# Kernel tuning notes

Measured on AMD Instinct MI355X. Metric: run time of the kernel, lower is better.

Reference implementation:

```python
import jax, jax.numpy as jnp
import numpy as np

B, N, S = 8, 8192, 2048
D1, D2 = 128, 256
IN_CH = D1 + D2  # 384
MLP = [256, 128]
BN_EPS = 1e-5


def setup_inputs() -> dict:
    key = jax.random.key(0)
    ks = jax.random.split(key, 12)
    inp = {
        'xyz1': jax.random.normal(ks[0], (B, 3, N), dtype=jnp.float32),
        'xyz2': jax.random.normal(ks[1], (B, 3, S), dtype=jnp.float32),
        'points1': jax.random.normal(ks[2], (B, D1, N), dtype=jnp.float32),
        'points2': jax.random.normal(ks[3], (B, D2, S), dtype=jnp.float32),
    }
    # Conv1d(kernel=1) weights [out, in] + bias, BN gamma/beta per layer
    c_in = IN_CH
    for i, c_out in enumerate(MLP):
        scale = 1.0 / np.sqrt(c_in)
        inp[f'w{i}'] = jax.random.uniform(ks[4 + 2 * i], (c_out, c_in), jnp.float32, -scale, scale)
        inp[f'b{i}'] = jax.random.uniform(ks[5 + 2 * i], (c_out,), jnp.float32, -scale, scale)
        inp[f'g{i}'] = jnp.ones((c_out,), jnp.float32)
        inp[f'be{i}'] = jnp.zeros((c_out,), jnp.float32)
        c_in = c_out
    return inp


def _fp_forward(xyz1, xyz2, points1, points2, params):
    # xyz1: [B,3,N] -> [B,N,3]; xyz2: [B,3,S] -> [B,S,3]
    p1 = jnp.transpose(xyz1, (0, 2, 1))
    p2 = jnp.transpose(xyz2, (0, 2, 1))
    # squared pairwise distances [B,N,S]
    dist = (jnp.sum(p1 * p1, -1)[:, :, None]
            + jnp.sum(p2 * p2, -1)[:, None, :]
            - 2.0 * jnp.einsum('bnc,bsc->bns', p1, p2))
    # 3 smallest distances per query point
    neg_d, idx = jax.lax.top_k(-dist, 3)          # idx: [B,N,3]
    d3 = -neg_d
    recip = 1.0 / (d3 + 1e-8)
    weight = recip / jnp.sum(recip, axis=2, keepdims=True)  # [B,N,3]
    # gather neighbor features: points2 [B,D2,S] -> [B,S,D2]
    feats = jnp.transpose(points2, (0, 2, 1))
    gathered = feats[jnp.arange(feats.shape[0])[:, None, None], idx]  # [B,N,3,D2]
    interp = jnp.einsum('bnkd,bnk->bdn', gathered, weight)            # [B,D2,N]
    x = jnp.concatenate([points1, interp], axis=1)                    # [B,D1+D2,N]
    # Conv1d(k=1) + BatchNorm1d(train-mode batch stats) + ReLU stack
    for w, b, g, be in params:
        x = jnp.einsum('oc,bcn->bon', w, x) + b[None, :, None]
        mean = jnp.mean(x, axis=(0, 2), keepdims=True)
        var = jnp.mean((x - mean) ** 2, axis=(0, 2), keepdims=True)
        x = (x - mean) * jax.lax.rsqrt(var + BN_EPS)
        x = x * g[None, :, None] + be[None, :, None]
        x = jax.nn.relu(x)
    return x


def reference(xyz1, xyz2, points1, points2, w0, b0, g0, be0, w1, b1, g1, be1):
    params = [(w0, b0, g0, be0), (w1, b1, g1, be1)]
    return _fp_forward(xyz1, xyz2, points1, points2, params)
```

## Files before the change

### kernel.cpp

```cpp
#include <hip/hip_runtime.h>

#define NB   8
#define NPT  8192
#define NS   2048
#define ND1  128
#define ND2  256
#define NIN  384
#define NC0  256
#define NC1  128
#define NBN  (NB*NPT)

typedef __bf16 bf16x8 __attribute__((ext_vector_type(8)));
typedef __bf16 bf16x4 __attribute__((ext_vector_type(4)));
typedef float  f32x4  __attribute__((ext_vector_type(4)));

#define SWZ(n, off) ((off) ^ (((n) & 7) << 4))

__global__ __launch_bounds__(256) void knn_kernel(
    const float* __restrict__ xyz1, const float* __restrict__ xyz2,
    int* __restrict__ idx3, float* __restrict__ wgt3)
{
    __shared__ float4 pts[NS];
    __shared__ float md[64][4][3];
    __shared__ int   mi[64][4][3];

    const int b  = blockIdx.x;
    const int qt = blockIdx.y;
    const float* x2 = xyz2 + (size_t)b * 3 * NS;
    for (int s = threadIdx.x; s < NS; s += 256) {
        float x = x2[s], y = x2[NS + s], z = x2[2 * NS + s];
        pts[s] = make_float4(x, y, z, x * x + y * y + z * z);
    }
    __syncthreads();

    const int q    = threadIdx.x & 63;
    const int part = threadIdx.x >> 6;
    const int n    = qt * 64 + q;
    const float* x1 = xyz1 + (size_t)b * 3 * NPT;
    const float px = x1[n], py = x1[NPT + n], pz = x1[2 * NPT + n];
    const float qx = -2.f * px, qy = -2.f * py, qz = -2.f * pz;

    float d0 = 3e38f, d1 = 3e38f, d2 = 3e38f;
    int   i0 = 0, i1 = 0, i2 = 0;
    const int sbeg = part * (NS / 4);
    #pragma unroll 2
    for (int s = sbeg; s < sbeg + NS / 4; ++s) {
        float4 p = pts[s];
        float d = fmaf(qx, p.x, fmaf(qy, p.y, fmaf(qz, p.z, p.w)));
        bool c0 = d < d0, c1 = d < d1, c2 = d < d2;
        i2 = c1 ? i1 : (c2 ? s : i2);
        i1 = c0 ? i0 : (c1 ? s : i1);
        i0 = c0 ? s  : i0;
        d2 = fminf(fmaxf(d, d1), d2);
        d1 = fminf(fmaxf(d, d0), d1);
        d0 = fminf(d, d0);
    }
    md[q][part][0] = d0; md[q][part][1] = d1; md[q][part][2] = d2;
    mi[q][part][0] = i0; mi[q][part][1] = i1; mi[q][part][2] = i2;
    __syncthreads();

    if (threadIdx.x < 64) {
        int hp[4] = {0, 0, 0, 0};
        float rd[3]; int ri[3];
        #pragma unroll
        for (int k = 0; k < 3; ++k) {
            float best = 3.0e38f; int bl = 0;
            #pragma unroll
            for (int l = 0; l < 4; ++l) {
                float dv = md[q][l][hp[l]];
                if (dv < best) { best = dv; bl = l; }
            }
            rd[k] = best; ri[k] = mi[q][bl][hp[bl]]; hp[bl]++;
        }
        const float p1sq = px * px + py * py + pz * pz;
        float r0 = 1.0f / (rd[0] + p1sq + 1e-8f);
        float r1 = 1.0f / (rd[1] + p1sq + 1e-8f);
        float r2 = 1.0f / (rd[2] + p1sq + 1e-8f);
        float inv = 1.0f / (r0 + r1 + r2);
        size_t base = ((size_t)b * NPT + n) * 3;
        idx3[base] = ri[0]; idx3[base + 1] = ri[1]; idx3[base + 2] = ri[2];
        wgt3[base] = r0 * inv; wgt3[base + 1] = r1 * inv; wgt3[base + 2] = r2 * inv;
    }
}

__global__ __launch_bounds__(256) void transpose_p2_kernel(
    const float* __restrict__ p2, __bf16* __restrict__ p2t)
{
    __shared__ float tile[64][65];
    const int b  = blockIdx.x;
    const int ts = (blockIdx.y & 31) * 64;
    const int td = (blockIdx.y >> 5) * 64;
    const int sl = threadIdx.x & 63, dl = threadIdx.x >> 6;
    #pragma unroll
    for (int i = 0; i < 16; ++i)
        tile[dl + 4 * i][sl] = p2[((size_t)b * ND2 + td + dl + 4 * i) * NS + ts + sl];
    __syncthreads();
    const int dl2 = threadIdx.x & 63, sl2 = threadIdx.x >> 6;
    #pragma unroll
    for (int i = 0; i < 16; ++i)
        p2t[((size_t)b * NS + ts + sl2 + 4 * i) * ND2 + td + dl2] =
            (__bf16)tile[dl2][sl2 + 4 * i];
}

__global__ __launch_bounds__(256) void transpose_p1_kernel(
    const float* __restrict__ p1, __bf16* __restrict__ XcP1)
{
    __shared__ float tile[64][65];
    const int b  = blockIdx.x;
    const int tn = (blockIdx.y & 127) * 64;
    const int tc = (blockIdx.y >> 7) * 64;
    const int sl = threadIdx.x & 63, dl = threadIdx.x >> 6;
    #pragma unroll
    for (int i = 0; i < 16; ++i)
        tile[dl + 4 * i][sl] = p1[((size_t)b * ND1 + tc + dl + 4 * i) * NPT + tn + sl];
    __syncthreads();
    const int n_local = threadIdx.x >> 2, c16 = threadIdx.x & 3;
    __bf16* dst = XcP1 + ((size_t)b * NPT + tn + n_local) * ND1 + tc + c16 * 16;
    bf16x8 v0, v1;
    #pragma unroll
    for (int k = 0; k < 8; ++k) {
        v0[k] = (__bf16)tile[c16 * 16 + k][n_local];
        v1[k] = (__bf16)tile[c16 * 16 + 8 + k][n_local];
    }
    *(bf16x8*)dst = v0;
    *(bf16x8*)(dst + 8) = v1;
}

__global__ __launch_bounds__(256) void convert_w_kernel(
    const float* __restrict__ w0, const float* __restrict__ w1,
    __bf16* __restrict__ Wb0, __bf16* __restrict__ Wb1)
{
    const int t = blockIdx.x * 256 + threadIdx.x;
    if (t < NC0 * NIN) Wb0[t] = (__bf16)w0[t];
    if (t < NC1 * NC0) Wb1[t] = (__bf16)w1[t];
}

__global__ __launch_bounds__(512, 4) void gemm0_fused(
    const __bf16* __restrict__ Wb, const __bf16* __restrict__ XcP1,
    const __bf16* __restrict__ p2t,
    const int* __restrict__ idx3, const float* __restrict__ wgt3,
    __bf16* __restrict__ y0, float* __restrict__ sums, float* __restrict__ sumsq)
{
    __shared__ char Bs[64 * ND2 * 2];
    __shared__ float red[2][NC0][2];

    const int tid = threadIdx.x;
    const int bn0 = blockIdx.x * 64;
    const int b   = bn0 / NPT;

    const int ng   = tid >> 3;
    const int part = tid & 7;
    const size_t base3 = (size_t)(bn0 + ng) * 3;
    const int gi0 = idx3[base3], gi1 = idx3[base3 + 1], gi2 = idx3[base3 + 2];
    const float gw0 = wgt3[base3], gw1 = wgt3[base3 + 1], gw2 = wgt3[base3 + 2];
    const __bf16* r0 = p2t + ((size_t)b * NS + gi0) * ND2;
    const __bf16* r1 = p2t + ((size_t)b * NS + gi1) * ND2;
    const __bf16* r2 = p2t + ((size_t)b * NS + gi2) * ND2;

    const int l = tid & 63, w = tid >> 6;
    const int g = l >> 4, lm = l & 15;
    const int ow = w >> 1, nw = w & 1;
    const int o_base = ow * 64;

    f32x4 acc[4][2] = {};

    bf16x8 rawA0, rawA1, rawA2, rawB0, rawB1, rawB2;
    {
        const int d0 = part * 32;
        rawA0 = *(const bf16x8*)(r0 + d0);     rawA1 = *(const bf16x8*)(r1 + d0);
        rawA2 = *(const bf16x8*)(r2 + d0);
        rawB0 = *(const bf16x8*)(r0 + d0 + 8); rawB1 = *(const bf16x8*)(r1 + d0 + 8);
        rawB2 = *(const bf16x8*)(r2 + d0 + 8);
    }

    #pragma unroll
    for (int k0 = 0; k0 < 64; k0 += 32) {
        const int kk = k0 + g * 8;
        bf16x8 af[4], bfr[2];
        #pragma unroll
        for (int m = 0; m < 4; ++m)
            af[m] = *(const bf16x8*)&Wb[(size_t)(o_base + m * 16 + lm) * NIN + kk];
        #pragma unroll
        for (int r = 0; r < 2; ++r) {
            const int n = nw * 32 + r * 16 + lm;
            bfr[r] = *(const bf16x8*)&XcP1[(size_t)(bn0 + n) * ND1 + kk];
        }
        #pragma unroll
        for (int m = 0; m < 4; ++m)
            #pragma unroll
            for (int r = 0; r < 2; ++r)
                acc[m][r] = __builtin_amdgcn_mfma_f32_16x16x32_bf16(af[m], bfr[r], acc[m][r], 0, 0, 0);
    }

    {
        bf16x8 v0, v1;
        #pragma unroll
        for (int j = 0; j < 8; ++j) {
            v0[j] = (__bf16)(gw0 * (float)rawA0[j] + gw1 * (float)rawA1[j] + gw2 * (float)rawA2[j]);
            v1[j] = (__bf16)(gw0 * (float)rawB0[j] + gw1 * (float)rawB1[j] + gw2 * (float)rawB2[j]);
        }
        const int d0 = part * 32;
        *(bf16x8*)(Bs + ng * (ND2 * 2) + SWZ(ng, d0 * 2))       = v0;
        *(bf16x8*)(Bs + ng * (ND2 * 2) + SWZ(ng, (d0 + 8) * 2)) = v1;
    }
    {
        const int d0 = part * 32 + 16;
        rawA0 = *(const bf16x8*)(r0 + d0);     rawA1 = *(const bf16x8*)(r1 + d0);
        rawA2 = *(const bf16x8*)(r2 + d0);
        rawB0 = *(const bf16x8*)(r0 + d0 + 8); rawB1 = *(const bf16x8*)(r1 + d0 + 8);
        rawB2 = *(const bf16x8*)(r2 + d0 + 8);
    }

    #pragma unroll
    for (int k0 = 64; k0 < 128; k0 += 32) {
        const int kk = k0 + g * 8;
        bf16x8 af[4], bfr[2];
        #pragma unroll
        for (int m = 0; m < 4; ++m)
            af[m] = *(const bf16x8*)&Wb[(size_t)(o_base + m * 16 + lm) * NIN + kk];
        #pragma unroll
        for (int r = 0; r < 2; ++r) {
            const int n = nw * 32 + r * 16 + lm;
            bfr[r] = *(const bf16x8*)&XcP1[(size_t)(bn0 + n) * ND1 + kk];
        }
        #pragma unroll
        for (int m = 0; m < 4; ++m)
            #pragma unroll
            for (int r = 0; r < 2; ++r)
                acc[m][r] = __builtin_amdgcn_mfma_f32_16x16x32_bf16(af[m], bfr[r], acc[m][r], 0, 0, 0);
    }

    {
        bf16x8 v0, v1;
        #pragma unroll
        for (int j = 0; j < 8; ++j) {
            v0[j] = (__bf16)(gw0 * (float)rawA0[j] + gw1 * (float)rawA1[j] + gw2 * (float)rawA2[j]);
            v1[j] = (__bf16)(gw0 * (float)rawB0[j] + gw1 * (float)rawB1[j] + gw2 * (float)rawB2[j]);
        }
        const int d0 = part * 32 + 16;
        *(bf16x8*)(Bs + ng * (ND2 * 2) + SWZ(ng, d0 * 2))       = v0;
        *(bf16x8*)(Bs + ng * (ND2 * 2) + SWZ(ng, (d0 + 8) * 2)) = v1;
    }
    __syncthreads();

    #pragma unroll
    for (int k0 = 128; k0 < NIN; k0 += 32) {
        const int kd = k0 - 128 + g * 8;
        bf16x8 af[4], bfr[2];
        #pragma unroll
        for (int m = 0; m < 4; ++m)
            af[m] = *(const bf16x8*)&Wb[(size_t)(o_base + m * 16 + lm) * NIN + k0 + g * 8];
        #pragma unroll
        for (int r = 0; r < 2; ++r) {
            const int n_lds = nw * 32 + r * 16 + lm;
            bfr[r] = *(const bf16x8*)(Bs + n_lds * (ND2 * 2) + SWZ(n_lds, kd * 2));
        }
        #pragma unroll
        for (int m = 0; m < 4; ++m)
            #pragma unroll
            for (int r = 0; r < 2; ++r)
                acc[m][r] = __builtin_amdgcn_mfma_f32_16x16x32_bf16(af[m], bfr[r], acc[m][r], 0, 0, 0);
    }

    #pragma unroll
    for (int m = 0; m < 4; ++m) {
        float s[4] = {0.f, 0.f, 0.f, 0.f}, q[4] = {0.f, 0.f, 0.f, 0.f};
        #pragma unroll
        for (int r = 0; r < 2; ++r) {
            const int n = nw * 32 + r * 16 + lm;
            bf16x4 pk;
            #pragma unroll
            for (int j = 0; j < 4; ++j) {
                float v = acc[m][r][j];
                pk[j] = (__bf16)v;
                s[j] += v; q[j] += v * v;
            }
            *(bf16x4*)&y0[(size_t)(bn0 + n) * NC0 + o_base + m * 16 + g * 4] = pk;
        }
        #pragma unroll
        for (int j = 0; j < 4; ++j) {
            #pragma unroll
            for (int st = 1; st < 16; st <<= 1) {
                s[j] += __shfl_xor(s[j], st);
                q[j] += __shfl_xor(q[j], st);
            }
        }
        if (lm == 0) {
            #pragma unroll
            for (int j = 0; j < 4; ++j) {
                red[0][o_base + m * 16 + g * 4 + j][nw] = s[j];
                red[1][o_base + m * 16 + g * 4 + j][nw] = q[j];
            }
        }
    }
    __syncthreads();
    if (tid < NC0) {
        atomicAdd(&sums[tid],  red[0][tid][0] + red[0][tid][1]);
        atomicAdd(&sumsq[tid], red[1][tid][0] + red[1][tid][1]);
    }
}

__global__ void stats_kernel(
    const float* __restrict__ sums, const float* __restrict__ sumsq,
    const float* __restrict__ g, const float* __restrict__ be,
    float* __restrict__ scale, float* __restrict__ shift, int C)
{
    int c = blockIdx.x * blockDim.x + threadIdx.x;
    if (c < C) {
        const float invN = 1.0f / (float)NBN;
        float mean = sums[c] * invN;
        float var  = sumsq[c] * invN - mean * mean;
        float sc   = g[c] * rsqrtf(var + 1e-5f);
        scale[c] = sc;
        shift[c] = be[c] - mean * sc;
    }
}

__global__ __launch_bounds__(512, 4) void gemm1_mfma(
    const __bf16* __restrict__ Wb, const __bf16* __restrict__ y0,
    const float* __restrict__ scale0, const float* __restrict__ shift0,
    __bf16* __restrict__ y1, float* __restrict__ sums, float* __restrict__ sumsq)
{
    __shared__ float red[2][NC1][4];
    const int tid = threadIdx.x;
    const int l = tid & 63, w = tid >> 6;
    const int g = l >> 4, lm = l & 15;
    const int ow = w >> 2, nw = w & 3;
    const int o_base = ow * 64;
    const int n_base = blockIdx.x * 128 + nw * 32;

    f32x4 acc[4][2] = {};

    for (int k0 = 0; k0 < NC0; k0 += 32) {
        const int kk = k0 + g * 8;
        f32x4 sc0 = *(const f32x4*)&scale0[kk];
        f32x4 sc1 = *(const f32x4*)&scale0[kk + 4];
        f32x4 sh0 = *(const f32x4*)&shift0[kk];
        f32x4 sh1 = *(const f32x4*)&shift0[kk + 4];
        bf16x8 af[4], bfr[2];
        #pragma unroll
        for (int m = 0; m < 4; ++m)
            af[m] = *(const bf16x8*)&Wb[(size_t)(o_base + m * 16 + lm) * NC0 + kk];
        #pragma unroll
        for (int r = 0; r < 2; ++r) {
            bf16x8 raw = *(const bf16x8*)&y0[(size_t)(n_base + r * 16 + lm) * NC0 + kk];
            bf16x8 bb;
            #pragma unroll
            for (int j = 0; j < 4; ++j) {
                bb[j]     = (__bf16)fmaxf((float)raw[j]     * sc0[j] + sh0[j], 0.f);
                bb[j + 4] = (__bf16)fmaxf((float)raw[j + 4] * sc1[j] + sh1[j], 0.f);
            }
            bfr[r] = bb;
        }
        #pragma unroll
        for (int m = 0; m < 4; ++m)
            #pragma unroll
            for (int r = 0; r < 2; ++r)
                acc[m][r] = __builtin_amdgcn_mfma_f32_16x16x32_bf16(af[m], bfr[r], acc[m][r], 0, 0, 0);
    }

    #pragma unroll
    for (int m = 0; m < 4; ++m) {
        float s[4] = {0.f, 0.f, 0.f, 0.f}, q[4] = {0.f, 0.f, 0.f, 0.f};
        #pragma unroll
        for (int r = 0; r < 2; ++r) {
            const int n = n_base + r * 16 + lm;
            #pragma unroll
            for (int j = 0; j < 4; ++j) {
                float v = acc[m][r][j];
                y1[(size_t)(o_base + m * 16 + g * 4 + j) * NBN + n] = (__bf16)v;
                s[j] += v; q[j] += v * v;
            }
        }
        #pragma unroll
        for (int j = 0; j < 4; ++j) {
            #pragma unroll
            for (int st = 1; st < 16; st <<= 1) {
                s[j] += __shfl_xor(s[j], st);
                q[j] += __shfl_xor(q[j], st);
            }
        }
        if (lm == 0) {
            #pragma unroll
            for (int j = 0; j < 4; ++j) {
                red[0][o_base + m * 16 + g * 4 + j][nw] = s[j];
                red[1][o_base + m * 16 + g * 4 + j][nw] = q[j];
            }
        }
    }
    __syncthreads();
    if (tid < NC1) {
        atomicAdd(&sums[tid],  red[0][tid][0] + red[0][tid][1] + red[0][tid][2] + red[0][tid][3]);
        atomicAdd(&sumsq[tid], red[1][tid][0] + red[1][tid][1] + red[1][tid][2] + red[1][tid][3]);
    }
}

__global__ __launch_bounds__(256) void bnout_kernel(
    const __bf16* __restrict__ y1, const float* __restrict__ scale1,
    const float* __restrict__ shift1, float* __restrict__ out)
{
    const size_t t = (size_t)blockIdx.x * 256 + threadIdx.x;
    const size_t e = t * 8;
    const int n = (int)(e & (NPT - 1));
    const int o = (int)((e >> 13) & (NC1 - 1));
    const int b = (int)(e >> 20);
    bf16x8 v = *(const bf16x8*)&y1[(size_t)o * NBN + (size_t)b * NPT + n];
    const float s = scale1[o], sh = shift1[o];
    f32x4 r0, r1;
    #pragma unroll
    for (int j = 0; j < 4; ++j) {
        r0[j] = fmaxf((float)v[j]     * s + sh, 0.f);
        r1[j] = fmaxf((float)v[j + 4] * s + sh, 0.f);
    }
    *(f32x4*)&out[e]     = r0;
    *(f32x4*)&out[e + 4] = r1;
}

extern "C" void kernel_launch(void* const* d_in, const int* in_sizes, int n_in,
                              void* d_out, int out_size, void* d_ws, size_t ws_size,
                              hipStream_t stream)
{
    const float* xyz1    = (const float*)d_in[0];
    const float* xyz2    = (const float*)d_in[1];
    const float* points1 = (const float*)d_in[2];
    const float* points2 = (const float*)d_in[3];
    const float* w0  = (const float*)d_in[4];
    const float* g0  = (const float*)d_in[6];
    const float* be0 = (const float*)d_in[7];
    const float* w1  = (const float*)d_in[8];
    const float* g1  = (const float*)d_in[10];
    const float* be1 = (const float*)d_in[11];

    char* ws = (char*)d_ws;
    size_t off = 0;
    int*    idx3 = (int*)(ws + off);    off += (size_t)NBN * 3 * 4;
    float*  wgt3 = (float*)(ws + off);  off += (size_t)NBN * 3 * 4;
    __bf16* XcP1 = (__bf16*)(ws + off); off += (size_t)NBN * ND1 * 2;
    __bf16* y0   = (__bf16*)(ws + off); off += (size_t)NBN * NC0 * 2;
    __bf16* y1   = (__bf16*)(ws + off); off += (size_t)NC1 * NBN * 2;
    __bf16* p2t  = (__bf16*)(ws + off); off += (size_t)NB * NS * ND2 * 2;
    __bf16* Wb0  = (__bf16*)(ws + off); off += (size_t)NC0 * NIN * 2;
    __bf16* Wb1  = (__bf16*)(ws + off); off += (size_t)NC1 * NC0 * 2;
    float*  stats = (float*)(ws + off);
    float* sums0  = stats;        float* sumsq0 = stats + 256;
    float* sums1  = stats + 512;  float* sumsq1 = stats + 640;
    float* scale0 = stats + 768;  float* shift0 = stats + 1024;
    float* scale1 = stats + 1280; float* shift1 = stats + 1408;

    hipMemsetAsync(stats, 0, 768 * 4, stream);

    convert_w_kernel   <<<dim3(NC0 * NIN / 256), 256, 0, stream>>>(w0, w1, Wb0, Wb1);
    transpose_p2_kernel<<<dim3(NB, 128), 256, 0, stream>>>(points2, p2t);
    transpose_p1_kernel<<<dim3(NB, 256), 256, 0, stream>>>(points1, XcP1);
    knn_kernel         <<<dim3(NB, 128), 256, 0, stream>>>(xyz1, xyz2, idx3, wgt3);
    gemm0_fused        <<<dim3(NBN / 64), 512, 0, stream>>>(
        Wb0, XcP1, p2t, idx3, wgt3, y0, sums0, sumsq0);
    stats_kernel       <<<1, 256, 0, stream>>>(sums0, sumsq0, g0, be0, scale0, shift0, NC0);
    gemm1_mfma         <<<dim3(NBN / 128), 512, 0, stream>>>(Wb1, y0, scale0, shift0, y1, sums1, sumsq1);
    stats_kernel       <<<1, 128, 0, stream>>>(sums1, sumsq1, g1, be1, scale1, shift1, NC1);
    bnout_kernel       <<<dim3(NBN * NC1 / 8 / 256), 256, 0, stream>>>(y1, scale1, shift1, (float*)d_out);
}
```

Before: 327.9 us.

## Pre-pack weights and activations into MFMA fragment-order layouts for coalesced loads

Weights, the transposed points1 and the layer-0 output are now written in a packed tile layout that matches the MFMA 16x16x32 operand fragment order. Each wavefront's fragment load then reads one contiguous 1KB chunk instead of 16 strided rows. The aim is to cut scattered global accesses and cache-line waste in both GEMMs. The cost is more complex index arithmetic in the producer kernels, and the packed y0 stores become more scattered.

```diff
diff --git a/kernel.cpp b/kernel.cpp
--- a/kernel.cpp
+++ b/kernel.cpp
@@ -15,6 +15,7 @@
 typedef float  f32x4  __attribute__((ext_vector_type(4)));
 
 #define SWZ(n, off) ((off) ^ (((n) & 7) << 4))
+
 
 __global__ __launch_bounds__(256) void knn_kernel(
     const float* __restrict__ xyz1, const float* __restrict__ xyz2,
@@ -103,7 +104,7 @@
 }
 
 __global__ __launch_bounds__(256) void transpose_p1_kernel(
-    const float* __restrict__ p1, __bf16* __restrict__ XcP1)
+    const float* __restrict__ p1, __bf16* __restrict__ Bp)
 {
     __shared__ float tile[64][65];
     const int b  = blockIdx.x;
@@ -115,37 +116,55 @@
         tile[dl + 4 * i][sl] = p1[((size_t)b * ND1 + tc + dl + 4 * i) * NPT + tn + sl];
     __syncthreads();
     const int n_local = threadIdx.x >> 2, c16 = threadIdx.x & 3;
-    __bf16* dst = XcP1 + ((size_t)b * NPT + tn + n_local) * ND1 + tc + c16 * 16;
     bf16x8 v0, v1;
     #pragma unroll
     for (int k = 0; k < 8; ++k) {
         v0[k] = (__bf16)tile[c16 * 16 + k][n_local];
         v1[k] = (__bf16)tile[c16 * 16 + 8 + k][n_local];
     }
-    *(bf16x8*)dst = v0;
-    *(bf16x8*)(dst + 8) = v1;
-}
-
-__global__ __launch_bounds__(256) void convert_w_kernel(
+    const int n16 = (int)(((size_t)b * NPT + tn + n_local) >> 4);
+    const int lm  = n_local & 15;
+    const int kc  = (tc >> 5) + (c16 >> 1);
+    const int g0  = (c16 & 1) * 2;
+    __bf16* base = Bp + (((size_t)n16 * 4 + kc) * 64 + lm) * 8;
+    *(bf16x8*)(base + g0 * 128)       = v0;
+    *(bf16x8*)(base + (g0 + 1) * 128) = v1;
+}
+
+__global__ __launch_bounds__(64) void pack_w_kernel(
     const float* __restrict__ w0, const float* __restrict__ w1,
-    __bf16* __restrict__ Wb0, __bf16* __restrict__ Wb1)
-{
-    const int t = blockIdx.x * 256 + threadIdx.x;
-    if (t < NC0 * NIN) Wb0[t] = (__bf16)w0[t];
-    if (t < NC1 * NC0) Wb1[t] = (__bf16)w1[t];
+    __bf16* __restrict__ Ap0, __bf16* __restrict__ Ap1)
+{
+    const int o  = blockIdx.x;
+    const int k8 = threadIdx.x;
+    if (k8 < 48) {
+        const float* src = w0 + (size_t)o * NIN + k8 * 8;
+        bf16x8 v;
+        #pragma unroll
+        for (int e = 0; e < 8; ++e) v[e] = (__bf16)src[e];
+        *(bf16x8*)&Ap0[((((o >> 4) * 12 + (k8 >> 2)) * 4 + (k8 & 3)) * 16 + (o & 15)) * 8] = v;
+    }
+    if (o < NC1 && k8 < 32) {
+        const float* src = w1 + (size_t)o * NC0 + k8 * 8;
+        bf16x8 v;
+        #pragma unroll
+        for (int e = 0; e < 8; ++e) v[e] = (__bf16)src[e];
+        *(bf16x8*)&Ap1[((((o >> 4) * 8 + (k8 >> 2)) * 4 + (k8 & 3)) * 16 + (o & 15)) * 8] = v;
+    }
 }
 
 __global__ __launch_bounds__(512, 4) void gemm0_fused(
-    const __bf16* __restrict__ Wb, const __bf16* __restrict__ XcP1,
+    const __bf16* __restrict__ Ap0, const __bf16* __restrict__ Bp,
     const __bf16* __restrict__ p2t,
     const int* __restrict__ idx3, const float* __restrict__ wgt3,
-    __bf16* __restrict__ y0, float* __restrict__ sums, float* __restrict__ sumsq)
+    __bf16* __restrict__ Yp, float* __restrict__ sums, float* __restrict__ sumsq)
 {
     __shared__ char Bs[64 * ND2 * 2];
     __shared__ float red[2][NC0][2];
 
     const int tid = threadIdx.x;
-    const int bn0 = blockIdx.x * 64;
+    const int bx  = blockIdx.x;
+    const int bn0 = bx * 64;
     const int b   = bn0 / NPT;
 
     const int ng   = tid >> 3;
@@ -175,16 +194,14 @@
 
     #pragma unroll
     for (int k0 = 0; k0 < 64; k0 += 32) {
-        const int kk = k0 + g * 8;
+        const int kc = k0 >> 5;
         bf16x8 af[4], bfr[2];
         #pragma unroll
         for (int m = 0; m < 4; ++m)
-            af[m] = *(const bf16x8*)&Wb[(size_t)(o_base + m * 16 + lm) * NIN + kk];
-        #pragma unroll
-        for (int r = 0; r < 2; ++r) {
-            const int n = nw * 32 + r * 16 + lm;
-            bfr[r] = *(const bf16x8*)&XcP1[(size_t)(bn0 + n) * ND1 + kk];
-        }
+            af[m] = *(const bf16x8*)&Ap0[(((ow * 4 + m) * 12 + kc) * 64 + l) * 8];
+        #pragma unroll
+        for (int r = 0; r < 2; ++r)
+            bfr[r] = *(const bf16x8*)&Bp[((((size_t)bx * 4 + nw * 2 + r) * 4 + kc) * 64 + l) * 8];
         #pragma unroll
         for (int m = 0; m < 4; ++m)
             #pragma unroll
@@ -213,16 +230,14 @@
 
     #pragma unroll
     for (int k0 = 64; k0 < 128; k0 += 32) {
-        const int kk = k0 + g * 8;
+        const int kc = k0 >> 5;
         bf16x8 af[4], bfr[2];
         #pragma unroll
         for (int m = 0; m < 4; ++m)
-            af[m] = *(const bf16x8*)&Wb[(size_t)(o_base + m * 16 + lm) * NIN + kk];
-        #pragma unroll
-        for (int r = 0; r < 2; ++r) {
-            const int n = nw * 32 + r * 16 + lm;
-            bfr[r] = *(const bf16x8*)&XcP1[(size_t)(bn0 + n) * ND1 + kk];
-        }
+            af[m] = *(const bf16x8*)&Ap0[(((ow * 4 + m) * 12 + kc) * 64 + l) * 8];
+        #pragma unroll
+        for (int r = 0; r < 2; ++r)
+            bfr[r] = *(const bf16x8*)&Bp[((((size_t)bx * 4 + nw * 2 + r) * 4 + kc) * 64 + l) * 8];
         #pragma unroll
         for (int m = 0; m < 4; ++m)
             #pragma unroll
@@ -245,11 +260,12 @@
 
     #pragma unroll
     for (int k0 = 128; k0 < NIN; k0 += 32) {
+        const int kc = k0 >> 5;
         const int kd = k0 - 128 + g * 8;
         bf16x8 af[4], bfr[2];
         #pragma unroll
         for (int m = 0; m < 4; ++m)
-            af[m] = *(const bf16x8*)&Wb[(size_t)(o_base + m * 16 + lm) * NIN + k0 + g * 8];
+            af[m] = *(const bf16x8*)&Ap0[(((ow * 4 + m) * 12 + kc) * 64 + l) * 8];
         #pragma unroll
         for (int r = 0; r < 2; ++r) {
             const int n_lds = nw * 32 + r * 16 + lm;
@@ -265,9 +281,11 @@
     #pragma unroll
     for (int m = 0; m < 4; ++m) {
         float s[4] = {0.f, 0.f, 0.f, 0.f}, q[4] = {0.f, 0.f, 0.f, 0.f};
+        const int kc = ow * 2 + (m >> 1);
+        const int g2 = (m & 1) * 2 + (g >> 1);
         #pragma unroll
         for (int r = 0; r < 2; ++r) {
-            const int n = nw * 32 + r * 16 + lm;
+            const int n16 = bx * 4 + nw * 2 + r;
             bf16x4 pk;
             #pragma unroll
             for (int j = 0; j < 4; ++j) {
@@ -275,7 +293,7 @@
                 pk[j] = (__bf16)v;
                 s[j] += v; q[j] += v * v;
             }
-            *(bf16x4*)&y0[(size_t)(bn0 + n) * NC0 + o_base + m * 16 + g * 4] = pk;
+            *(bf16x4*)&Yp[(((size_t)n16 * 8 + kc) * 64 + g2 * 16 + lm) * 8 + (g & 1) * 4] = pk;
         }
         #pragma unroll
         for (int j = 0; j < 4; ++j) {
@@ -317,21 +335,23 @@
 }
 
 __global__ __launch_bounds__(512, 4) void gemm1_mfma(
-    const __bf16* __restrict__ Wb, const __bf16* __restrict__ y0,
+    const __bf16* __restrict__ Ap1, const __bf16* __restrict__ Yp,
     const float* __restrict__ scale0, const float* __restrict__ shift0,
     __bf16* __restrict__ y1, float* __restrict__ sums, float* __restrict__ sumsq)
 {
     __shared__ float red[2][NC1][4];
     const int tid = threadIdx.x;
+    const int bx  = blockIdx.x;
     const int l = tid & 63, w = tid >> 6;
     const int g = l >> 4, lm = l & 15;
     const int ow = w >> 2, nw = w & 3;
     const int o_base = ow * 64;
-    const int n_base = blockIdx.x * 128 + nw * 32;
+    const int n_base = bx * 128 + nw * 32;
 
     f32x4 acc[4][2] = {};
 
     for (int k0 = 0; k0 < NC0; k0 += 32) {
+        const int kc = k0 >> 5;
         const int kk = k0 + g * 8;
         f32x4 sc0 = *(const f32x4*)&scale0[kk];
         f32x4 sc1 = *(const f32x4*)&scale0[kk + 4];
@@ -340,10 +360,10 @@
         bf16x8 af[4], bfr[2];
         #pragma unroll
         for (int m = 0; m < 4; ++m)
-            af[m] = *(const bf16x8*)&Wb[(size_t)(o_base + m * 16 + lm) * NC0 + kk];
+            af[m] = *(const bf16x8*)&Ap1[(((ow * 4 + m) * 8 + kc) * 64 + l) * 8];
         #pragma unroll
         for (int r = 0; r < 2; ++r) {
-            bf16x8 raw = *(const bf16x8*)&y0[(size_t)(n_base + r * 16 + lm) * NC0 + kk];
+            bf16x8 raw = *(const bf16x8*)&Yp[((((size_t)bx * 8 + nw * 2 + r) * 8 + kc) * 64 + l) * 8];
             bf16x8 bb;
             #pragma unroll
             for (int j = 0; j < 4; ++j) {
@@ -435,12 +455,12 @@
     size_t off = 0;
     int*    idx3 = (int*)(ws + off);    off += (size_t)NBN * 3 * 4;
     float*  wgt3 = (float*)(ws + off);  off += (size_t)NBN * 3 * 4;
-    __bf16* XcP1 = (__bf16*)(ws + off); off += (size_t)NBN * ND1 * 2;
-    __bf16* y0   = (__bf16*)(ws + off); off += (size_t)NBN * NC0 * 2;
+    __bf16* Bp   = (__bf16*)(ws + off); off += (size_t)NBN * ND1 * 2;
+    __bf16* Yp   = (__bf16*)(ws + off); off += (size_t)NBN * NC0 * 2;
     __bf16* y1   = (__bf16*)(ws + off); off += (size_t)NC1 * NBN * 2;
     __bf16* p2t  = (__bf16*)(ws + off); off += (size_t)NB * NS * ND2 * 2;
-    __bf16* Wb0  = (__bf16*)(ws + off); off += (size_t)NC0 * NIN * 2;
-    __bf16* Wb1  = (__bf16*)(ws + off); off += (size_t)NC1 * NC0 * 2;
+    __bf16* Ap0  = (__bf16*)(ws + off); off += (size_t)NC0 * NIN * 2;
+    __bf16* Ap1  = (__bf16*)(ws + off); off += (size_t)NC1 * NC0 * 2;
     float*  stats = (float*)(ws + off);
     float* sums0  = stats;        float* sumsq0 = stats + 256;
     float* sums1  = stats + 512;  float* sumsq1 = stats + 640;
@@ -449,14 +469,14 @@
 
     hipMemsetAsync(stats, 0, 768 * 4, stream);
 
-    convert_w_kernel   <<<dim3(NC0 * NIN / 256), 256, 0, stream>>>(w0, w1, Wb0, Wb1);
+    pack_w_kernel      <<<dim3(NC0), 64, 0, stream>>>(w0, w1, Ap0, Ap1);
     transpose_p2_kernel<<<dim3(NB, 128), 256, 0, stream>>>(points2, p2t);
-    transpose_p1_kernel<<<dim3(NB, 256), 256, 0, stream>>>(points1, XcP1);
+    transpose_p1_kernel<<<dim3(NB, 256), 256, 0, stream>>>(points1, Bp);
     knn_kernel         <<<dim3(NB, 128), 256, 0, stream>>>(xyz1, xyz2, idx3, wgt3);
     gemm0_fused        <<<dim3(NBN / 64), 512, 0, stream>>>(
-        Wb0, XcP1, p2t, idx3, wgt3, y0, sums0, sumsq0);
+        Ap0, Bp, p2t, idx3, wgt3, Yp, sums0, sumsq0);
     stats_kernel       <<<1, 256, 0, stream>>>(sums0, sumsq0, g0, be0, scale0, shift0, NC0);
-    gemm1_mfma         <<<dim3(NBN / 128), 512, 0, stream>>>(Wb1, y0, scale0, shift0, y1, sums1, sumsq1);
+    gemm1_mfma         <<<dim3(NBN / 128), 512, 0, stream>>>(Ap1, Yp, scale0, shift0, y1, sums1, sumsq1);
     stats_kernel       <<<1, 128, 0, stream>>>(sums1, sumsq1, g1, be1, scale1, shift1, NC1);
     bnout_kernel       <<<dim3(NBN * NC1 / 8 / 256), 256, 0, stream>>>(y1, scale1, shift1, (float*)d_out);
 }
```

Result: faster. 291.5 us (-11.1%).
